# Performance work log

Hardware: AMD Instinct MI355X
Metric: run time of the kernel (lower is better)

Reference implementation:

```python
import jax, jax.numpy as jnp
import numpy as np

B, T, F, H = 512, 512, 64, 64  # batch, time, input feat, hidden


def setup_inputs() -> dict:
    key = jax.random.key(0)
    k1, k2, k3, k4 = jax.random.split(key, 4)
    ins = jax.random.normal(k1, (B, T, F), jnp.float32)
    resets = jax.random.randint(k2, (B, T), 0, 2).astype(bool)
    # Flax LSTMCell: 4 input->hidden dense (no bias) + 4 hidden->hidden dense (bias),
    # concatenated here as [i, f, g, o] blocks of width H.
    si = 1.0 / np.sqrt(F)
    sh = 1.0 / np.sqrt(H)
    Wi = jax.random.uniform(k3, (F, 4 * H), jnp.float32, -si, si)
    Wh = jax.random.uniform(k4, (H, 4 * H), jnp.float32, -sh, sh)
    b = jnp.zeros((4 * H,), jnp.float32)
    return {"ins": ins, "resets": resets, "Wi": Wi, "Wh": Wh, "b": b}


def reference(ins, resets, Wi, Wh, b):
    Bn, Tn, _ = ins.shape
    Hn = Wh.shape[0]

    def step(carry, xt):
        c, h = carry
        x_t, r_t = xt  # x_t: [B, F], r_t: [B]
        m = r_t[:, None]
        c = jnp.where(m, 0.0, c)  # reset to initialize_carry (zeros)
        h = jnp.where(m, 0.0, h)
        z = x_t @ Wi + h @ Wh + b  # [B, 4H]
        i, f, g, o = jnp.split(z, 4, axis=-1)
        i = jax.nn.sigmoid(i)
        f = jax.nn.sigmoid(f)
        g = jnp.tanh(g)
        o = jax.nn.sigmoid(o)
        c_new = f * c + i * g
        h_new = o * jnp.tanh(c_new)
        return (c_new, h_new), h_new

    c0 = jnp.zeros((Bn, Hn), ins.dtype)
    h0 = jnp.zeros((Bn, Hn), ins.dtype)
    xs = (jnp.swapaxes(ins, 0, 1), jnp.swapaxes(resets, 0, 1))  # time-major
    _, ys = jax.lax.scan(step, (c0, h0), xs)
    return jnp.swapaxes(ys, 0, 1)  # [B, T, H]
```

## Files before the change

### kernel.cpp

```cpp
#include <hip/hip_runtime.h>


#define NB 512
#define NT 512
#define NF 64
#define NH 64
#define NG 256
#define TCHUNK 32

__device__ __forceinline__ float rcp_fast(float x) { return __builtin_amdgcn_rcpf(x); }
__device__ __forceinline__ float sig_fast(float x) { return rcp_fast(1.0f + __expf(-x)); }
__device__ __forceinline__ float tanh_fast(float x) {
    return 1.0f - 2.0f * rcp_fast(1.0f + __expf(2.0f * x));
}

__global__ void detect_resets_dtype(const unsigned int* __restrict__ r, int n,
                                    int* __restrict__ flag) {
    int bits = 0;
    for (int i = blockIdx.x * blockDim.x + threadIdx.x; i < n;
         i += gridDim.x * blockDim.x) {
        unsigned v = r[i];
        if (v == 0x3F800000u) bits |= 2;
        else if (v != 0u && v != 1u) bits |= 4;
    }
    if (bits) atomicOr(flag, bits);
}

__global__ __launch_bounds__(256, 2)
void lstm_scan_kernel(const float* __restrict__ ins, const void* __restrict__ resets,
                      const float* __restrict__ Wi, const float* __restrict__ Wh,
                      const float* __restrict__ bias, float* __restrict__ out,
                      const int* __restrict__ flag) {
    const int b = blockIdx.x;
    const int j = threadIdx.x;

    int mode = 0;
    if (flag) {
        int fl = *flag;
        if ((fl & 2) && !(fl & 4)) mode = 2;
        else if (fl & 4) mode = 1;
    }

    float wi[NF], wh[NF];
#pragma unroll
    for (int k = 0; k < NF; ++k) {
        wi[k] = Wi[k * NG + j];
        wh[k] = Wh[k * NG + j];
    }
    const float bj = bias[j];

    __shared__ __align__(16) float xs[TCHUNK][NF];
    __shared__ int rs[TCHUNK];
    __shared__ __align__(16) float hbuf[2][NH];
    __shared__ float zbuf[NG];

    float c = 0.0f;
    if (j < NH) { hbuf[0][j] = 0.0f; hbuf[1][j] = 0.0f; }
    __syncthreads();

    int cur = 0;
    for (int t0 = 0; t0 < NT; t0 += TCHUNK) {
        {
            const float4* src = (const float4*)(ins + ((size_t)b * NT + t0) * NF);
            float4* dst = (float4*)&xs[0][0];
            dst[j] = src[j];
            dst[j + 256] = src[j + 256];
            if (j < TCHUNK) {
                int idx = b * NT + t0 + j;
                int rv;
                if (mode == 1)      rv = ((const unsigned char*)resets)[idx] != 0;
                else if (mode == 2) rv = ((const float*)resets)[idx] != 0.0f;
                else                rv = ((const int*)resets)[idx] != 0;
                rs[j] = rv;
            }
        }
        __syncthreads();

        for (int tt = 0; tt < TCHUNK; ++tt) {
            const int t = t0 + tt;
            const int rst = rs[tt];

            float accx = bj;
            float acch = 0.0f;
            const float4* xv4 = (const float4*)&xs[tt][0];
#pragma unroll
            for (int k4 = 0; k4 < NF / 4; ++k4) {
                float4 xv = xv4[k4];
                accx = fmaf(xv.x, wi[4 * k4 + 0], accx);
                accx = fmaf(xv.y, wi[4 * k4 + 1], accx);
                accx = fmaf(xv.z, wi[4 * k4 + 2], accx);
                accx = fmaf(xv.w, wi[4 * k4 + 3], accx);
            }
            if (!rst) {
                const float4* hv4 = (const float4*)&hbuf[cur][0];
#pragma unroll
                for (int k4 = 0; k4 < NF / 4; ++k4) {
                    float4 hv = hv4[k4];
                    acch = fmaf(hv.x, wh[4 * k4 + 0], acch);
                    acch = fmaf(hv.y, wh[4 * k4 + 1], acch);
                    acch = fmaf(hv.z, wh[4 * k4 + 2], acch);
                    acch = fmaf(hv.w, wh[4 * k4 + 3], acch);
                }
            }
            zbuf[j] = accx + acch;
            __syncthreads();

            if (j < NH) {
                float zi = zbuf[j];
                float zf = zbuf[j + NH];
                float zg = zbuf[j + 2 * NH];
                float zo = zbuf[j + 3 * NH];
                float ig = sig_fast(zi);
                float fg = sig_fast(zf);
                float gg = tanh_fast(zg);
                float og = sig_fast(zo);
                float cc = rst ? 0.0f : c;
                cc = fg * cc + ig * gg;
                c = cc;
                float hh = og * tanh_fast(cc);
                hbuf[cur ^ 1][j] = hh;
                out[((size_t)b * NT + t) * NH + j] = hh;
            }
            __syncthreads();
            cur ^= 1;
        }
    }
}

extern "C" void kernel_launch(void* const* d_in, const int* in_sizes, int n_in,
                              void* d_out, int out_size, void* d_ws, size_t ws_size,
                              hipStream_t stream) {
    const float* ins    = (const float*)d_in[0];
    const void*  resets = d_in[1];
    const float* Wi     = (const float*)d_in[2];
    const float* Wh     = (const float*)d_in[3];
    const float* bias   = (const float*)d_in[4];
    float* out = (float*)d_out;

    int* flag = nullptr;
    if (d_ws && ws_size >= sizeof(int)) {
        flag = (int*)d_ws;
        hipMemsetAsync(flag, 0, sizeof(int), stream);
        detect_resets_dtype<<<256, 256, 0, stream>>>(
            (const unsigned int*)resets, NB * NT, flag);
    }

    lstm_scan_kernel<<<NB, 256, 0, stream>>>(ins, resets, Wi, Wh, bias, out, flag);
}
```

Baseline: 495.8 us.

## Split LSTM into bf16 MFMA input GEMM and reset-segmented recurrence

Precomputes the input projection x@Wi+b for all timesteps with a bf16 MFMA GEMM into a workspace buffer. It then builds a list of reset-delimited segments so that independent segments can be processed in parallel by waves, each wave interleaving four segments. One wave handles all four gates per hidden unit, with Wh kept in registers. This removes the serial per-batch scan over all 512 steps and the block-wide barriers, but adds bf16 rounding of Z and inputs, a large workspace requirement, and atomics-based list building.

```diff
diff --git a/kernel.cpp b/kernel.cpp
--- a/kernel.cpp
+++ b/kernel.cpp
@@ -1,5 +1,9 @@
 #include <hip/hip_runtime.h>
-
+#include <hip/hip_bf16.h>
+
+
+typedef __attribute__((ext_vector_type(8))) short short8;
+typedef __attribute__((ext_vector_type(4))) float f32x4;
 
 #define NB 512
 #define NT 512
@@ -7,11 +11,20 @@
 #define NH 64
 #define NG 256
 #define TCHUNK 32
+#define NWAVES 2048
 
 __device__ __forceinline__ float rcp_fast(float x) { return __builtin_amdgcn_rcpf(x); }
 __device__ __forceinline__ float sig_fast(float x) { return rcp_fast(1.0f + __expf(-x)); }
 __device__ __forceinline__ float tanh_fast(float x) {
     return 1.0f - 2.0f * rcp_fast(1.0f + __expf(2.0f * x));
+}
+__device__ __forceinline__ unsigned pkbf(float a, float b) {
+    __hip_bfloat162 h = __float22bfloat162_rn(make_float2(a, b));
+    unsigned u; __builtin_memcpy(&u, &h, 4); return u;
+}
+__device__ __forceinline__ unsigned short f2bf(float x) {
+    unsigned u = __float_as_uint(x);
+    return (unsigned short)((u + 0x7FFFu + ((u >> 16) & 1u)) >> 16);
 }
 
 __global__ void detect_resets_dtype(const unsigned int* __restrict__ r, int n,
@@ -25,6 +38,206 @@
     }
     if (bits) atomicOr(flag, bits);
 }
+__device__ __forceinline__ int decode_mode(const int* flag) {
+    int fl = *flag;
+    if ((fl & 2) && !(fl & 4)) return 2;
+    if (fl & 4) return 1;
+    return 0;
+}
+__device__ __forceinline__ int load_rst(const void* resets, int mode, long idx) {
+    if (mode == 1) return ((const unsigned char*)resets)[idx] != 0;
+    if (mode == 2) return ((const float*)resets)[idx] != 0.0f;
+    return ((const int*)resets)[idx] != 0;
+}
+
+__global__ __launch_bounds__(64)
+void seg_build(const void* __restrict__ resets, const int* __restrict__ flag,
+               unsigned* __restrict__ list, int* __restrict__ cnt) {
+    const int b = blockIdx.x;
+    const int tid = threadIdx.x;
+    const int mode = decode_mode(flag);
+    __shared__ unsigned char r[NT];
+#pragma unroll
+    for (int i = 0; i < NT / 64; ++i)
+        r[tid + 64 * i] = (unsigned char)load_rst(resets, mode, (long)b * NT + tid + 64 * i);
+    __syncthreads();
+#pragma unroll
+    for (int i = 0; i < NT / 64; ++i) {
+        const int t = tid + 64 * i;
+        if (t == 0 || r[t]) {
+            int e = t + 1;
+            while (e < NT && !r[e]) ++e;
+            const int idx = atomicAdd(cnt, 1);
+            list[idx] = ((unsigned)b << 19) | ((unsigned)t << 10) | (unsigned)(e - t);
+        }
+    }
+}
+
+__global__ __launch_bounds__(256, 2)
+void zgemm3(const float* __restrict__ ins, const float* __restrict__ Wi,
+            const float* __restrict__ bias, unsigned short* __restrict__ Z) {
+    const int tid = threadIdx.x;
+    const int lane = tid & 63;
+    const int w = tid >> 6;
+    const int l15 = lane & 15, l4 = lane >> 4;
+    const long bt0 = (long)blockIdx.x * 64;
+    const int pbase = w << 6;
+
+    __shared__ __align__(16) unsigned short xs[64][72];
+
+    {
+        const float4* src = (const float4*)(ins + bt0 * NF);
+#pragma unroll
+        for (int i = 0; i < 4; ++i) {
+            const int q = tid + 256 * i;
+            const int row = q >> 4, c4 = (q & 15) << 2;
+            const float4 v = src[q];
+            *(uint2*)&xs[row][c4] = make_uint2(pkbf(v.x, v.y), pkbf(v.z, v.w));
+        }
+    }
+
+    short8 afr[4][2];
+    f32x4 binit[4];
+#pragma unroll
+    for (int pt = 0; pt < 4; ++pt) {
+        const int prow = pbase + pt * 16 + l15;
+        const int n = (prow & 3) * 64 + (prow >> 2);
+#pragma unroll
+        for (int kc = 0; kc < 2; ++kc) {
+            union { unsigned u[4]; short8 s; } cv;
+#pragma unroll
+            for (int e2 = 0; e2 < 4; ++e2) {
+                const int k = kc * 32 + l4 * 8 + e2 * 2;
+                cv.u[e2] = pkbf(Wi[k * NG + n], Wi[(k + 1) * NG + n]);
+            }
+            afr[pt][kc] = cv.s;
+        }
+        f32x4 bi;
+#pragma unroll
+        for (int r = 0; r < 4; ++r) {
+            const int pr = pbase + pt * 16 + l4 * 4 + r;
+            bi[r] = bias[(pr & 3) * 64 + (pr >> 2)];
+        }
+        binit[pt] = bi;
+    }
+    __syncthreads();
+
+#pragma unroll
+    for (int tt = 0; tt < 4; ++tt) {
+        short8 bfr[2];
+#pragma unroll
+        for (int kc = 0; kc < 2; ++kc)
+            bfr[kc] = *(const short8*)&xs[tt * 16 + l15][kc * 32 + l4 * 8];
+        const long bt = bt0 + tt * 16 + l15;
+#pragma unroll
+        for (int pt = 0; pt < 4; ++pt) {
+            f32x4 acc = binit[pt];
+            acc = __builtin_amdgcn_mfma_f32_16x16x32_bf16(afr[pt][0], bfr[0], acc, 0, 0, 0);
+            acc = __builtin_amdgcn_mfma_f32_16x16x32_bf16(afr[pt][1], bfr[1], acc, 0, 0, 0);
+            const int p0 = pbase + pt * 16 + l4 * 4;
+            *(uint2*)&Z[bt * NG + p0] =
+                make_uint2(pkbf(acc[0], acc[1]), pkbf(acc[2], acc[3]));
+        }
+    }
+}
+
+__global__ __launch_bounds__(256, 1)
+void lstm_recur3(const uint2* __restrict__ Z2, const float* __restrict__ Wh,
+                 float* __restrict__ out, const unsigned* __restrict__ list,
+                 const int* __restrict__ cnt) {
+    const int tid = threadIdx.x;
+    const int j = tid & 63;
+    const int wv = __builtin_amdgcn_readfirstlane(tid >> 6);
+    const int wid = __builtin_amdgcn_readfirstlane((int)blockIdx.x * 4 + (tid >> 6));
+    const int nseg = __builtin_amdgcn_readfirstlane(*cnt);
+
+    float whi[NF], whf[NF], whg[NF], who[NF];
+#pragma unroll
+    for (int k = 0; k < NF; ++k) {
+        whi[k] = Wh[k * NG + j];
+        whf[k] = Wh[k * NG + NH + j];
+        whg[k] = Wh[k * NG + 2 * NH + j];
+        who[k] = Wh[k * NG + 3 * NH + j];
+    }
+
+    __shared__ __align__(16) float hls[4][4][NH];
+
+    int qi = wid;
+    long ob0, ob1, ob2, ob3;
+    int rem0 = 0, rem1 = 0, rem2 = 0, rem3 = 0;
+    int act0 = 0, act1 = 0, act2 = 0, act3 = 0;
+    int fr0 = 0, fr1 = 0, fr2 = 0, fr3 = 0;
+    float c0 = 0, c1 = 0, c2 = 0, c3 = 0;
+    uint2 zz0, zz1, zz2, zz3;
+
+#define POP(S) do {                                                            \
+        if (qi < nseg) {                                                       \
+            const unsigned sg = __builtin_amdgcn_readfirstlane(list[qi]);      \
+            qi += NWAVES;                                                      \
+            const int sb = (int)(sg >> 19);                                    \
+            const int st = (int)((sg >> 10) & 511u);                           \
+            rem##S = (int)(sg & 1023u);                                        \
+            ob##S = ((long)sb * NT + st) * 64;                                 \
+            zz##S = Z2[ob##S + j];                                             \
+            act##S = 1; fr##S = 1; c##S = 0.0f;                                \
+        } else { act##S = 0; }                                                 \
+    } while (0)
+
+#define STEP(S) do {                                                           \
+        float si = __uint_as_float(zz##S.x << 16);                             \
+        float sf = __uint_as_float(zz##S.x & 0xFFFF0000u);                     \
+        float sg_ = __uint_as_float(zz##S.y << 16);                            \
+        float so = __uint_as_float(zz##S.y & 0xFFFF0000u);                     \
+        if (!fr##S) {                                                          \
+            const f32x4* hp = (const f32x4*)&hls[wv][S][0];                    \
+            _Pragma("unroll")                                                  \
+            for (int q = 0; q < 16; ++q) {                                     \
+                const f32x4 hv = hp[q];                                        \
+                si = fmaf(hv[0], whi[4 * q + 0], si);                          \
+                si = fmaf(hv[1], whi[4 * q + 1], si);                          \
+                si = fmaf(hv[2], whi[4 * q + 2], si);                          \
+                si = fmaf(hv[3], whi[4 * q + 3], si);                          \
+                sf = fmaf(hv[0], whf[4 * q + 0], sf);                          \
+                sf = fmaf(hv[1], whf[4 * q + 1], sf);                          \
+                sf = fmaf(hv[2], whf[4 * q + 2], sf);                          \
+                sf = fmaf(hv[3], whf[4 * q + 3], sf);                          \
+                sg_ = fmaf(hv[0], whg[4 * q + 0], sg_);                        \
+                sg_ = fmaf(hv[1], whg[4 * q + 1], sg_);                        \
+                sg_ = fmaf(hv[2], whg[4 * q + 2], sg_);                        \
+                sg_ = fmaf(hv[3], whg[4 * q + 3], sg_);                        \
+                so = fmaf(hv[0], who[4 * q + 0], so);                          \
+                so = fmaf(hv[1], who[4 * q + 1], so);                          \
+                so = fmaf(hv[2], who[4 * q + 2], so);                          \
+                so = fmaf(hv[3], who[4 * q + 3], so);                          \
+            }                                                                  \
+        }                                                                      \
+        const float ig = sig_fast(si);                                         \
+        const float fg = sig_fast(sf);                                         \
+        const float gg = tanh_fast(sg_);                                       \
+        const float og = sig_fast(so);                                         \
+        c##S = fr##S ? (ig * gg) : fmaf(fg, c##S, ig * gg);                    \
+        const float hh = og * tanh_fast(c##S);                                 \
+        out[ob##S + j] = hh;                                                   \
+        hls[wv][S][j] = hh;                                                    \
+        ob##S += 64;                                                           \
+        if (--rem##S > 0) zz##S = Z2[ob##S + j]; else act##S = 0;              \
+        fr##S = 0;                                                             \
+    } while (0)
+
+    for (;;) {
+        if (!act0) POP(0);
+        if (!act1) POP(1);
+        if (!act2) POP(2);
+        if (!act3) POP(3);
+        if (!(act0 | act1 | act2 | act3)) break;
+        if (act0) STEP(0);
+        if (act1) STEP(1);
+        if (act2) STEP(2);
+        if (act3) STEP(3);
+    }
+#undef POP
+#undef STEP
+}
 
 __global__ __launch_bounds__(256, 2)
 void lstm_scan_kernel(const float* __restrict__ ins, const void* __restrict__ resets,
@@ -33,13 +246,7 @@
                       const int* __restrict__ flag) {
     const int b = blockIdx.x;
     const int j = threadIdx.x;
-
-    int mode = 0;
-    if (flag) {
-        int fl = *flag;
-        if ((fl & 2) && !(fl & 4)) mode = 2;
-        else if (fl & 4) mode = 1;
-    }
+    int mode = flag ? decode_mode(flag) : 0;
 
     float wi[NF], wh[NF];
 #pragma unroll
@@ -65,23 +272,14 @@
             float4* dst = (float4*)&xs[0][0];
             dst[j] = src[j];
             dst[j + 256] = src[j + 256];
-            if (j < TCHUNK) {
-                int idx = b * NT + t0 + j;
-                int rv;
-                if (mode == 1)      rv = ((const unsigned char*)resets)[idx] != 0;
-                else if (mode == 2) rv = ((const float*)resets)[idx] != 0.0f;
-                else                rv = ((const int*)resets)[idx] != 0;
-                rs[j] = rv;
-            }
+            if (j < TCHUNK) rs[j] = load_rst(resets, mode, (long)b * NT + t0 + j);
         }
         __syncthreads();
 
         for (int tt = 0; tt < TCHUNK; ++tt) {
             const int t = t0 + tt;
             const int rst = rs[tt];
-
-            float accx = bj;
-            float acch = 0.0f;
+            float accx = bj, acch = 0.0f;
             const float4* xv4 = (const float4*)&xs[tt][0];
 #pragma unroll
             for (int k4 = 0; k4 < NF / 4; ++k4) {
@@ -104,16 +302,9 @@
             }
             zbuf[j] = accx + acch;
             __syncthreads();
-
             if (j < NH) {
-                float zi = zbuf[j];
-                float zf = zbuf[j + NH];
-                float zg = zbuf[j + 2 * NH];
-                float zo = zbuf[j + 3 * NH];
-                float ig = sig_fast(zi);
-                float fg = sig_fast(zf);
-                float gg = tanh_fast(zg);
-                float og = sig_fast(zo);
+                float zi = zbuf[j], zf = zbuf[j + NH], zg = zbuf[j + 2 * NH], zo = zbuf[j + 3 * NH];
+                float ig = sig_fast(zi), fg = sig_fast(zf), gg = tanh_fast(zg), og = sig_fast(zo);
                 float cc = rst ? 0.0f : c;
                 cc = fg * cc + ig * gg;
                 c = cc;
@@ -137,13 +328,30 @@
     const float* bias   = (const float*)d_in[4];
     float* out = (float*)d_out;
 
-    int* flag = nullptr;
-    if (d_ws && ws_size >= sizeof(int)) {
-        flag = (int*)d_ws;
-        hipMemsetAsync(flag, 0, sizeof(int), stream);
-        detect_resets_dtype<<<256, 256, 0, stream>>>(
-            (const unsigned int*)resets, NB * NT, flag);
-    }
-
-    lstm_scan_kernel<<<NB, 256, 0, stream>>>(ins, resets, Wi, Wh, bias, out, flag);
-}
+    const int nBT = NB * NT;
+    const size_t ZBF16   = (size_t)nBT * NG * 2;
+    const size_t METAOFF = ZBF16;
+    const size_t LISTOFF = ZBF16 + 64;
+    const size_t NEEDED  = LISTOFF + (size_t)nBT * 4 + 64;
+
+    if (ws_size >= NEEDED) {
+        unsigned short* Z = (unsigned short*)d_ws;
+        int* flag = (int*)((char*)d_ws + METAOFF);
+        int* cnt  = flag + 1;
+        unsigned* list = (unsigned*)((char*)d_ws + LISTOFF);
+
+        hipMemsetAsync(flag, 0, 8, stream);
+        detect_resets_dtype<<<256, 256, 0, stream>>>((const unsigned int*)resets, nBT, flag);
+        seg_build<<<NB, 64, 0, stream>>>(resets, flag, list, cnt);
+        zgemm3<<<nBT / 64, 256, 0, stream>>>(ins, Wi, bias, Z);
+        lstm_recur3<<<NWAVES / 4, 256, 0, stream>>>((const uint2*)Z, Wh, out, list, cnt);
+    } else {
+        int* flag = nullptr;
+        if (d_ws && ws_size >= sizeof(int)) {
+            flag = (int*)d_ws;
+            hipMemsetAsync(flag, 0, sizeof(int), stream);
+            detect_resets_dtype<<<256, 256, 0, stream>>>((const unsigned int*)resets, nBT, flag);
+        }
+        lstm_scan_kernel<<<NB, 256, 0, stream>>>(ins, resets, Wi, Wh, bias, out, flag);
+    }
+}
```

Result: slower. 517.4 us (+4.4%).
